# Performance work log

Measured on AMD Instinct MI355X. Metric: run time of the kernel, lower is better.

## Reference

```python
import jax, jax.numpy as jnp
import numpy as np

B, L, C = 256, 196, 768      # batch, tokens (14x14 grid), token_dim
K = 2048                      # codebook size (num_tokens)
H = W = 14                    # h = int(sqrt(L)), w = L // h


def setup_inputs() -> dict:
    key = jax.random.key(0)
    k1, k2, k3 = jax.random.split(key, 3)
    in_feas = jax.random.normal(k1, (B, L, C), dtype=jnp.float32)
    codebook = jax.random.normal(k2, (K, C), dtype=jnp.float32)
    # Conv1d(in=C, out=1, kernel=3, padding=1, bias=False) weight: [1, C, 3]
    att_w = jax.random.normal(k3, (1, C, 3), dtype=jnp.float32) * 0.02
    return {"in_feas": in_feas, "codebook": codebook, "att_w": att_w}


def reference(in_feas, codebook, att_w):
    b, l, c = in_feas.shape
    flat = in_feas.reshape(-1, c)  # [B*L, C]

    # --- SOHO visual-dictionary (VQ) nearest-neighbour lookup ---
    d = (jnp.sum(flat * flat, axis=1, keepdims=True)
         - 2.0 * flat @ codebook.T
         + jnp.sum(codebook * codebook, axis=1)[None, :])  # [B*L, K]
    encoding_indices = jnp.argmin(d, axis=1)               # [B*L] int
    quantized = codebook[encoding_indices]                 # [B*L, C]
    # straight-through estimator: output = x + sg(q - x)
    vd_outputs = flat + jax.lax.stop_gradient(quantized - flat)

    idx_out = encoding_indices.reshape(-1, H, W)

    # --- attention branch (att=True, not_plus=False) ---
    # Conv1d(C->1, k=3, pad=1) applied to each token as a length-1 sequence:
    # only the center tap att_w[0, :, 1] multiplies real data (neighbors are
    # zero padding), so the conv reduces to a dot with the center weights.
    att = jax.nn.relu(vd_outputs @ att_w[0, :, 1])         # [B*L]
    att_mask = jax.nn.softmax(att.reshape(b, l, 1), axis=1)  # softmax over L

    vd_outputs = vd_outputs.reshape(b, l, c)
    out_feas = vd_outputs + in_feas * att_mask
    return out_feas, idx_out
```

## Files before the change

### kernel.cpp

```cpp
#include <hip/hip_runtime.h>

#define B_ 256
#define L_ 196
#define C_ 768
#define K_ 2048
#define BL_ 50176

typedef __attribute__((ext_vector_type(8))) short bf16x8;
typedef __attribute__((ext_vector_type(4))) float f32x4;

typedef const __attribute__((address_space(1))) void gas_void;
typedef __attribute__((address_space(3))) void las_void;

__device__ __forceinline__ unsigned short f2bf(float f) {
  unsigned u = __builtin_bit_cast(unsigned, f);
  u = u + 0x7FFFu + ((u >> 16) & 1u);
  return (unsigned short)(u >> 16);
}

__device__ __forceinline__ unsigned fmono(float f) {
  unsigned u = __builtin_bit_cast(unsigned, f);
  return u ^ ((unsigned)((int)u >> 31) | 0x80000000u);
}

__global__ __launch_bounds__(256) void precompute_kernel(
    const float* __restrict__ cb, const float* __restrict__ attw,
    unsigned short* __restrict__ cbb, double* __restrict__ norms64,
    float* __restrict__ norms32, float* __restrict__ ac) {
  int wave = threadIdx.x >> 6;
  int lane = threadIdx.x & 63;
  int k = blockIdx.x * 4 + wave;
  const float* row = cb + (size_t)k * C_;
  double n = 0.0, a = 0.0;
  for (int c = lane; c < C_; c += 64) {
    float v = row[c];
    cbb[(size_t)k * C_ + c] = f2bf(v);
    n = fma((double)v, (double)v, n);
    a = fma((double)v, (double)attw[c * 3 + 1], a);
  }
  for (int off = 32; off > 0; off >>= 1) {
    n += __shfl_down(n, off);
    a += __shfl_down(a, off);
  }
  if (lane == 0) {
    norms64[k] = n;
    norms32[k] = (float)n;
    ac[k] = (a > 0.0) ? (float)a : 0.0f;
  }
}

__global__ __launch_bounds__(256) void convert_kernel(
    const float* __restrict__ x, unsigned short* __restrict__ xb) {
  int i = blockIdx.x * 256 + threadIdx.x;
  float4 v = ((const float4*)x)[i];
  uint2 w;
  w.x = (unsigned)f2bf(v.x) | ((unsigned)f2bf(v.y) << 16);
  w.y = (unsigned)f2bf(v.z) | ((unsigned)f2bf(v.w) << 16);
  ((uint2*)xb)[i] = w;
}

__global__ __launch_bounds__(512, 2) void phase1_kernel(
    const unsigned short* __restrict__ xb,
    const unsigned short* __restrict__ cbb,
    const float* __restrict__ norms32, unsigned* __restrict__ ws_cand) {
  __shared__ unsigned short lds[2][2][2][128 * 64];
  __shared__ float norms_s[256];
  __shared__ unsigned cands_s[256][12];

  int tid = threadIdx.x;
  int bid = blockIdx.x;
  int x8 = bid & 7, m = bid >> 3;
  int mblk, nblk;
  if (m < 192) {
    mblk = (m & ~7) | x8;
    nblk = m & 7;
  } else {
    mblk = m;
    nblk = x8;
  }
  size_t row0 = (size_t)mblk * 256;
  int code0 = nblk * 256;

  int wv = tid >> 6, l = tid & 63;
  int wm = wv >> 2, wn = wv & 3;
  int col16 = l & 15, quad = l >> 4;

  if (tid < 256) norms_s[tid] = norms32[code0 + tid];

  int slotraw = (tid & 7) ^ ((tid >> 3) & 7);
  const unsigned short* abase = xb + (row0 + (tid >> 3)) * (size_t)C_ +
                                (size_t)slotraw * 8;
  const unsigned short* bbase = cbb + ((size_t)code0 + (tid >> 3)) * C_ +
                                (size_t)slotraw * 8;

  auto stageA = [&](int kt, int half, int buf) {
    const unsigned short* s =
        abase + (size_t)half * 128 * C_ + (size_t)kt * 64;
    char* d = (char*)&lds[buf][0][half][0] + wv * 1024;
    __builtin_amdgcn_global_load_lds((gas_void*)s, (las_void*)d, 16, 0, 0);
    __builtin_amdgcn_global_load_lds((gas_void*)(s + (size_t)64 * C_),
                                     (las_void*)(d + 8192), 16, 0, 0);
  };
  auto stageB = [&](int kt, int half, int buf) {
    const unsigned short* s =
        bbase + (size_t)half * 128 * C_ + (size_t)kt * 64;
    char* d = (char*)&lds[buf][1][half][0] + wv * 1024;
    __builtin_amdgcn_global_load_lds((gas_void*)s, (las_void*)d, 16, 0, 0);
    __builtin_amdgcn_global_load_lds((gas_void*)(s + (size_t)64 * C_),
                                     (las_void*)(d + 8192), 16, 0, 0);
  };

  f32x4 acc[2][2][4][2];
#pragma unroll
  for (int mh = 0; mh < 2; ++mh)
#pragma unroll
    for (int nh = 0; nh < 2; ++nh)
#pragma unroll
      for (int mt = 0; mt < 4; ++mt)
#pragma unroll
        for (int nt = 0; nt < 2; ++nt)
          acc[mh][nh][mt][nt] = (f32x4){0.f, 0.f, 0.f, 0.f};

  bf16x8 af[4][2], bfr[2][2];

#define LOADA(P)                                                            \
  _Pragma("unroll") for (int mt = 0; mt < 4; ++mt)                          \
      _Pragma("unroll") for (int ks = 0; ks < 2; ++ks) af[mt][ks] =         \
      *(const bf16x8*)((P) + (wm * 64 + mt * 16 + col16) * 128 +            \
                       (((ks * 4 + quad) ^ (col16 & 7)) * 16));

#define LOADB(P)                                                            \
  _Pragma("unroll") for (int nt = 0; nt < 2; ++nt)                          \
      _Pragma("unroll") for (int ks = 0; ks < 2; ++ks) bfr[nt][ks] =        \
      *(const bf16x8*)((P) + (wn * 32 + nt * 16 + col16) * 128 +            \
                       (((ks * 4 + quad) ^ (col16 & 7)) * 16));

#define MFMA_PHASE(mh, nh)                                                  \
  __builtin_amdgcn_s_barrier();                                             \
  asm volatile("s_waitcnt lgkmcnt(0)" ::: "memory");                        \
  __builtin_amdgcn_s_setprio(1);                                            \
  _Pragma("unroll") for (int mt = 0; mt < 4; ++mt)                          \
      _Pragma("unroll") for (int nt = 0; nt < 2; ++nt)                      \
          _Pragma("unroll") for (int ks = 0; ks < 2; ++ks) acc[mh][nh][mt]  \
      [nt] = __builtin_amdgcn_mfma_f32_16x16x32_bf16(                       \
          af[mt][ks], bfr[nt][ks], acc[mh][nh][mt][nt], 0, 0, 0);           \
  __builtin_amdgcn_s_setprio(0);                                            \
  __builtin_amdgcn_s_barrier();

  stageA(0, 0, 0);
  stageB(0, 1, 0);
  stageA(0, 1, 0);
  stageB(0, 0, 0);
  stageA(1, 0, 1);
  stageB(1, 1, 1);
  stageA(1, 1, 1);
  asm volatile("s_waitcnt vmcnt(6)" ::: "memory");
  __builtin_amdgcn_s_barrier();

  for (int kt = 0; kt < 12; ++kt) {
    int buf = kt & 1;
    const char* A0p = (const char*)&lds[buf][0][0][0];
    const char* A1p = (const char*)&lds[buf][0][1][0];
    const char* B0p = (const char*)&lds[buf][1][0][0];
    const char* B1p = (const char*)&lds[buf][1][1][0];

    if (kt + 1 < 12) stageB(kt + 1, 0, buf ^ 1);
    LOADA(A0p);
    LOADB(B0p);
    MFMA_PHASE(0, 0);
    if (kt + 2 < 12) stageA(kt + 2, 0, buf);
    LOADB(B1p);
    MFMA_PHASE(0, 1);
    if (kt + 2 < 12) stageB(kt + 2, 1, buf);
    LOADA(A1p);
    MFMA_PHASE(1, 1);
    if (kt + 2 < 12) stageA(kt + 2, 1, buf);
    if (kt <= 9) {
      asm volatile("s_waitcnt vmcnt(6)" ::: "memory");
    } else if (kt == 10) {
      asm volatile("s_waitcnt vmcnt(0)" ::: "memory");
    }
    LOADB(B0p);
    MFMA_PHASE(1, 0);
  }

#undef LOADA
#undef LOADB
#undef MFMA_PHASE

#pragma unroll
  for (int mh = 0; mh < 2; ++mh) {
#pragma unroll
    for (int mt = 0; mt < 4; ++mt) {
#pragma unroll
      for (int r = 0; r < 4; ++r) {
        unsigned keys[4];
#pragma unroll
        for (int nh = 0; nh < 2; ++nh)
#pragma unroll
          for (int nt = 0; nt < 2; ++nt) {
            int codel = nh * 128 + wn * 32 + nt * 16 + col16;
            float d = fmaf(-2.0f, acc[mh][nh][mt][nt][r], norms_s[codel]);
            keys[nh * 2 + nt] =
                (fmono(d) & 0xFFFFF800u) | (unsigned)(code0 + codel);
          }
        unsigned win[3];
#pragma unroll
        for (int rnd = 0; rnd < 3; ++rnd) {
          unsigned mn = min(min(keys[0], keys[1]), min(keys[2], keys[3]));
          mn = min(mn, (unsigned)__shfl_xor((int)mn, 1));
          mn = min(mn, (unsigned)__shfl_xor((int)mn, 2));
          mn = min(mn, (unsigned)__shfl_xor((int)mn, 4));
          mn = min(mn, (unsigned)__shfl_xor((int)mn, 8));
          win[rnd] = mn;
#pragma unroll
          for (int nt = 0; nt < 4; ++nt)
            if (keys[nt] == mn) keys[nt] = 0xFFFFFFFFu;
        }
        if (col16 == 0) {
          int t = mh * 128 + wm * 64 + mt * 16 + quad * 4 + r;
          cands_s[t][wn * 3 + 0] = win[0];
          cands_s[t][wn * 3 + 1] = win[1];
          cands_s[t][wn * 3 + 2] = win[2];
        }
      }
    }
  }
  __syncthreads();
  for (int i = tid; i < 256 * 12; i += 512) {
    int t = i / 12;
    int j = i - t * 12;
    ws_cand[(row0 + t) * 96 + nblk * 12 + j] = cands_s[t][j];
  }
}

__global__ __launch_bounds__(256) void phase2_kernel(
    const float* __restrict__ x, const float* __restrict__ cb,
    const unsigned* __restrict__ ws_cand, const double* __restrict__ norms64,
    int* __restrict__ out_idx) {
  __shared__ unsigned cl[32][100];
  __shared__ int rcode[32][6];
  __shared__ double rd[32][6];
  int tid = threadIdx.x;
  size_t tok0 = (size_t)blockIdx.x * 32;

  for (int i = tid; i < 32 * 96; i += 256) {
    int t = i / 96;
    int s = i - t * 96;
    cl[t][s] = ws_cand[tok0 * 96 + i];
  }
  __syncthreads();

  if (tid < 32) {
    unsigned best[6];
#pragma unroll
    for (int j = 0; j < 6; ++j) best[j] = 0xFFFFFFFFu;
    for (int s = 0; s < 96; ++s) {
      unsigned v = cl[tid][s];
      if (v < best[5]) {
        best[5] = v;
#pragma unroll
        for (int j = 5; j > 0; --j) {
          if (best[j] < best[j - 1]) {
            unsigned t = best[j];
            best[j] = best[j - 1];
            best[j - 1] = t;
          }
        }
      }
    }
#pragma unroll
    for (int j = 0; j < 6; ++j) rcode[tid][j] = (int)(best[j] & 0x7FFu);
  }
  __syncthreads();

  if (tid < 192) {
    int t = tid / 6;
    int j = tid - t * 6;
    int code = rcode[t][j];
    const float* xr = x + (tok0 + t) * (size_t)C_;
    const float* cr = cb + (size_t)code * C_;
    double s = 0.0;
    for (int c = 0; c < C_; c += 4) {
      float4 xa = *(const float4*)(xr + c);
      float4 ca = *(const float4*)(cr + c);
      s = fma((double)xa.x, (double)ca.x, s);
      s = fma((double)xa.y, (double)ca.y, s);
      s = fma((double)xa.z, (double)ca.z, s);
      s = fma((double)xa.w, (double)ca.w, s);
    }
    rd[t][j] = fma(-2.0, s, norms64[code]);
  }
  __syncthreads();

  if (tid < 32) {
    double bv = rd[tid][0];
    int bi = rcode[tid][0];
#pragma unroll
    for (int j = 1; j < 6; ++j) {
      double v = rd[tid][j];
      int i0 = rcode[tid][j];
      if (v < bv || (v == bv && i0 < bi)) {
        bv = v;
        bi = i0;
      }
    }
    out_idx[tok0 + tid] = bi;
  }
}

#define APAD 776
__global__ __launch_bounds__(256, 2) void argmin_fallback(
    const float* __restrict__ x, const float* __restrict__ cb,
    const unsigned short* __restrict__ cbb,
    const double* __restrict__ norms64, const float* __restrict__ norms32,
    int* __restrict__ out_idx) {
  __shared__ unsigned short Asf[32 * APAD];
  __shared__ float norms_s[K_];
  __shared__ unsigned int cands[32][48];
  __shared__ int rcode[32][6];
  __shared__ double rd[32][6];

  int tid = threadIdx.x;
  size_t tok0 = (size_t)blockIdx.x * 32;

  for (int i = tid; i < K_; i += 256) norms_s[i] = norms32[i];

  const float4* xin = (const float4*)(x + tok0 * C_);
  for (int i = tid; i < 32 * 192; i += 256) {
    int tok = i / 192;
    int c4 = i - tok * 192;
    float4 v = xin[i];
    uint2 w;
    w.x = (unsigned)f2bf(v.x) | ((unsigned)f2bf(v.y) << 16);
    w.y = (unsigned)f2bf(v.z) | ((unsigned)f2bf(v.w) << 16);
    *(uint2*)&Asf[tok * APAD + c4 * 4] = w;
  }
  __syncthreads();

  int wv = tid >> 6;
  int lane = tid & 63;
  int col = lane & 15;
  int quad = lane >> 4;

  const unsigned short* a0p = &Asf[(col)*APAD + quad * 8];
  const unsigned short* a1p = &Asf[(16 + col) * APAD + quad * 8];

  for (int chunk = 0; chunk < 4; ++chunk) {
    int code0 = chunk * 512 + wv * 128 + col;
    const unsigned short* bbase = cbb + (size_t)code0 * C_ + quad * 8;

    f32x4 acc[2][8];
#pragma unroll
    for (int m = 0; m < 2; ++m)
#pragma unroll
      for (int n = 0; n < 8; ++n) acc[m][n] = (f32x4){0.f, 0.f, 0.f, 0.f};

    bf16x8 ca0 = *(const bf16x8*)(a0p);
    bf16x8 ca1 = *(const bf16x8*)(a1p);
    bf16x8 cbf[8];
#pragma unroll
    for (int n = 0; n < 8; ++n)
      cbf[n] = *(const bf16x8*)(bbase + (size_t)n * 16 * C_);

    for (int ks = 0; ks < 24; ++ks) {
      bf16x8 na0, na1, nbf[8];
      if (ks < 23) {
        int k1 = (ks + 1) * 32;
        na0 = *(const bf16x8*)(a0p + k1);
        na1 = *(const bf16x8*)(a1p + k1);
#pragma unroll
        for (int n = 0; n < 8; ++n)
          nbf[n] = *(const bf16x8*)(bbase + (size_t)n * 16 * C_ + k1);
      }
#pragma unroll
      for (int n = 0; n < 8; ++n) {
        acc[0][n] = __builtin_amdgcn_mfma_f32_16x16x32_bf16(ca0, cbf[n],
                                                            acc[0][n], 0, 0, 0);
        acc[1][n] = __builtin_amdgcn_mfma_f32_16x16x32_bf16(ca1, cbf[n],
                                                            acc[1][n], 0, 0, 0);
      }
      if (ks < 23) {
        ca0 = na0;
        ca1 = na1;
#pragma unroll
        for (int n = 0; n < 8; ++n) cbf[n] = nbf[n];
      }
    }

#pragma unroll
    for (int m = 0; m < 2; ++m) {
#pragma unroll
      for (int r = 0; r < 4; ++r) {
        unsigned keys[8];
#pragma unroll
        for (int n = 0; n < 8; ++n) {
          int code = code0 + n * 16;
          float d = fmaf(-2.0f, acc[m][n][r], norms_s[code]);
          keys[n] = (fmono(d) & 0xFFFFF800u) | (unsigned)code;
        }
        unsigned win[3];
#pragma unroll
        for (int rnd = 0; rnd < 3; ++rnd) {
          unsigned mn = keys[0];
#pragma unroll
          for (int n = 1; n < 8; ++n) mn = min(mn, keys[n]);
          mn = min(mn, (unsigned)__shfl_xor((int)mn, 1));
          mn = min(mn, (unsigned)__shfl_xor((int)mn, 2));
          mn = min(mn, (unsigned)__shfl_xor((int)mn, 4));
          mn = min(mn, (unsigned)__shfl_xor((int)mn, 8));
          win[rnd] = mn;
#pragma unroll
          for (int n = 0; n < 8; ++n)
            if (keys[n] == mn) keys[n] = 0xFFFFFFFFu;
        }
        if (col == 0) {
          int token = m * 16 + quad * 4 + r;
          unsigned* cp = &cands[token][chunk * 12 + wv * 3];
          cp[0] = win[0];
          cp[1] = win[1];
          cp[2] = win[2];
        }
      }
    }
  }
  __syncthreads();

  if (tid < 32) {
    unsigned best[6];
#pragma unroll
    for (int j = 0; j < 6; ++j) best[j] = 0xFFFFFFFFu;
    for (int s = 0; s < 48; ++s) {
      unsigned v = cands[tid][s];
      if (v < best[5]) {
        best[5] = v;
#pragma unroll
        for (int j = 5; j > 0; --j) {
          if (best[j] < best[j - 1]) {
            unsigned t = best[j];
            best[j] = best[j - 1];
            best[j - 1] = t;
          }
        }
      }
    }
#pragma unroll
    for (int j = 0; j < 6; ++j) rcode[tid][j] = (int)(best[j] & 0x7FFu);
  }
  __syncthreads();

  if (tid < 192) {
    int t = tid / 6;
    int j = tid - t * 6;
    int code = rcode[t][j];
    const float* xr = x + (tok0 + t) * (size_t)C_;
    const float* cr = cb + (size_t)code * C_;
    double s = 0.0;
    for (int c = 0; c < C_; c += 4) {
      float4 xa = *(const float4*)(xr + c);
      float4 ca = *(const float4*)(cr + c);
      s = fma((double)xa.x, (double)ca.x, s);
      s = fma((double)xa.y, (double)ca.y, s);
      s = fma((double)xa.z, (double)ca.z, s);
      s = fma((double)xa.w, (double)ca.w, s);
    }
    rd[t][j] = fma(-2.0, s, norms64[code]);
  }
  __syncthreads();

  if (tid < 32) {
    double bv = rd[tid][0];
    int bi = rcode[tid][0];
#pragma unroll
    for (int j = 1; j < 6; ++j) {
      double v = rd[tid][j];
      int i0 = rcode[tid][j];
      if (v < bv || (v == bv && i0 < bi)) {
        bv = v;
        bi = i0;
      }
    }
    out_idx[tok0 + tid] = bi;
  }
}

__global__ __launch_bounds__(1024) void epilogue_kernel(
    const float* __restrict__ x, const float* __restrict__ cb,
    const float* __restrict__ ac, const int* __restrict__ idx,
    float* __restrict__ out, float* __restrict__ out_idx) {
  __shared__ float att[256];
  __shared__ float red[256];
  __shared__ int ids[L_];
  int b = blockIdx.x;
  int tid = threadIdx.x;

  float e = 0.0f;
  if (tid < 256) {
    float a = -1e30f;
    if (tid < L_) {
      int myid = idx[b * L_ + tid];
      ids[tid] = myid;
      a = ac[myid];
    }
    att[tid] = a;
    red[tid] = a;
  }
  __syncthreads();
  for (int s = 128; s > 0; s >>= 1) {
    if (tid < s) red[tid] = fmaxf(red[tid], red[tid + s]);
    __syncthreads();
  }
  float mx = red[0];
  __syncthreads();
  if (tid < 256) {
    e = (tid < L_) ? expf(att[tid] - mx) : 0.0f;
    red[tid] = e;
  }
  __syncthreads();
  for (int s = 128; s > 0; s >>= 1) {
    if (tid < s) red[tid] += red[tid + s];
    __syncthreads();
  }
  float sum = red[0];
  __syncthreads();
  if (tid < 256) att[tid] = e / sum;
  __syncthreads();

  const float4* xin = (const float4*)(x + (size_t)b * L_ * C_);
  float4* o = (float4*)(out + (size_t)b * L_ * C_);
  for (int i = tid; i < L_ * (C_ / 4); i += 1024) {
    int l = i / (C_ / 4);
    int c4 = i - l * (C_ / 4);
    const float4* crow = (const float4*)(cb + (size_t)ids[l] * C_);
    float4 xv = xin[i];
    float4 cv = crow[c4];
    float mk = att[l];
    float4 ov;
    ov.x = cv.x + xv.x * mk;
    ov.y = cv.y + xv.y * mk;
    ov.z = cv.z + xv.z * mk;
    ov.w = cv.w + xv.w * mk;
    o[i] = ov;
  }
  if (tid < L_) out_idx[b * L_ + tid] = (float)ids[tid];
}

extern "C" void kernel_launch(void* const* d_in, const int* in_sizes, int n_in,
                              void* d_out, int out_size, void* d_ws,
                              size_t ws_size, hipStream_t stream) {
  const float* in_feas = (const float*)d_in[0];
  const float* cb = (const float*)d_in[1];
  const float* attw = (const float*)d_in[2];

  char* ws = (char*)d_ws;
  size_t off = 0;
  unsigned short* cbb = (unsigned short*)(ws + off); off += 3145728;
  double* norms64 = (double*)(ws + off);           off += 16384;
  float* norms32 = (float*)(ws + off);             off += 8192;
  float* ac = (float*)(ws + off);                  off += 8192;
  int* idx = (int*)(ws + off);                     off += 200704;
  size_t base = off;
  unsigned short* xb = (unsigned short*)(ws + off); off += (size_t)BL_ * C_ * 2;
  unsigned* ws_cand = (unsigned*)(ws + off);        off += (size_t)BL_ * 96 * 4;
  size_t need_full = off;

  float* out = (float*)d_out;
  float* out_idx = out + (size_t)B_ * L_ * C_;

  precompute_kernel<<<K_ / 4, 256, 0, stream>>>(cb, attw, cbb, norms64,
                                                norms32, ac);
  if (ws_size >= need_full) {
    convert_kernel<<<BL_ * C_ / 4 / 256, 256, 0, stream>>>(in_feas, xb);
    phase1_kernel<<<dim3((BL_ / 256) * (K_ / 256)), 512, 0, stream>>>(
        xb, cbb, norms32, ws_cand);
    phase2_kernel<<<BL_ / 32, 256, 0, stream>>>(in_feas, cb, ws_cand, norms64,
                                                idx);
  } else {
    argmin_fallback<<<BL_ / 32, 256, 0, stream>>>(in_feas, cb, cbb, norms64,
                                                  norms32, idx);
  }
  epilogue_kernel<<<B_, 1024, 0, stream>>>(in_feas, cb, ac, idx, out, out_idx);
  (void)base;
}
```

Measured before the change: 796.4 us.

## Restructure GEMM K-loop pipeline with one-stage prefetch and fewer barriers

Result: faster. 777.9 us (-2.3%).

```diff
diff --git a/kernel.cpp b/kernel.cpp
--- a/kernel.cpp
+++ b/kernel.cpp
@@ -135,58 +135,68 @@
       *(const bf16x8*)((P) + (wn * 32 + nt * 16 + col16) * 128 +            \
                        (((ks * 4 + quad) ^ (col16 & 7)) * 16));
 
-#define MFMA_PHASE(mh, nh)                                                  \
-  __builtin_amdgcn_s_barrier();                                             \
-  asm volatile("s_waitcnt lgkmcnt(0)" ::: "memory");                        \
+#define MFMA_Q(mh, nh)                                                      \
   __builtin_amdgcn_s_setprio(1);                                            \
   _Pragma("unroll") for (int mt = 0; mt < 4; ++mt)                          \
       _Pragma("unroll") for (int nt = 0; nt < 2; ++nt)                      \
           _Pragma("unroll") for (int ks = 0; ks < 2; ++ks) acc[mh][nh][mt]  \
       [nt] = __builtin_amdgcn_mfma_f32_16x16x32_bf16(                       \
           af[mt][ks], bfr[nt][ks], acc[mh][nh][mt][nt], 0, 0, 0);           \
-  __builtin_amdgcn_s_setprio(0);                                            \
-  __builtin_amdgcn_s_barrier();
+  __builtin_amdgcn_s_setprio(0);
 
   stageA(0, 0, 0);
+  stageB(0, 0, 0);
   stageB(0, 1, 0);
   stageA(0, 1, 0);
-  stageB(0, 0, 0);
-  stageA(1, 0, 1);
-  stageB(1, 1, 1);
-  stageA(1, 1, 1);
-  asm volatile("s_waitcnt vmcnt(6)" ::: "memory");
+  asm volatile("s_waitcnt vmcnt(4)" ::: "memory");
   __builtin_amdgcn_s_barrier();
 
-  for (int kt = 0; kt < 12; ++kt) {
-    int buf = kt & 1;
+  for (int t = 0; t < 12; ++t) {
+    int buf = t & 1;
     const char* A0p = (const char*)&lds[buf][0][0][0];
     const char* A1p = (const char*)&lds[buf][0][1][0];
     const char* B0p = (const char*)&lds[buf][1][0][0];
     const char* B1p = (const char*)&lds[buf][1][1][0];
-
-    if (kt + 1 < 12) stageB(kt + 1, 0, buf ^ 1);
+    bool st = (t < 11);
+
+    if (st) {
+      stageA(t + 1, 0, buf ^ 1);
+      stageB(t + 1, 0, buf ^ 1);
+    }
     LOADA(A0p);
     LOADB(B0p);
-    MFMA_PHASE(0, 0);
-    if (kt + 2 < 12) stageA(kt + 2, 0, buf);
+    MFMA_Q(0, 0);
+    if (st) {
+      asm volatile("s_waitcnt vmcnt(6)" ::: "memory");
+    } else {
+      asm volatile("s_waitcnt vmcnt(2)" ::: "memory");
+    }
+    __builtin_amdgcn_s_barrier();
+
+    if (st) stageB(t + 1, 1, buf ^ 1);
     LOADB(B1p);
-    MFMA_PHASE(0, 1);
-    if (kt + 2 < 12) stageB(kt + 2, 1, buf);
+    MFMA_Q(0, 1);
+    if (st) {
+      asm volatile("s_waitcnt vmcnt(6)" ::: "memory");
+    } else {
+      asm volatile("s_waitcnt vmcnt(0)" ::: "memory");
+    }
+    __builtin_amdgcn_s_barrier();
+
+    if (st) stageA(t + 1, 1, buf ^ 1);
     LOADA(A1p);
-    MFMA_PHASE(1, 1);
-    if (kt + 2 < 12) stageA(kt + 2, 1, buf);
-    if (kt <= 9) {
-      asm volatile("s_waitcnt vmcnt(6)" ::: "memory");
-    } else if (kt == 10) {
-      asm volatile("s_waitcnt vmcnt(0)" ::: "memory");
-    }
+    MFMA_Q(1, 1);
     LOADB(B0p);
-    MFMA_PHASE(1, 0);
+    MFMA_Q(1, 0);
+    if (st) {
+      asm volatile("s_waitcnt vmcnt(4)" ::: "memory");
+    }
+    __builtin_amdgcn_s_barrier();
   }
 
 #undef LOADA
 #undef LOADB
-#undef MFMA_PHASE
+#undef MFMA_Q
 
 #pragma unroll
   for (int mh = 0; mh < 2; ++mh) {
```
